# Optimization experiments

Measured on AMD Instinct MI355X. Metric: run time of the kernel, lower is better.

Reference implementation:

```python
import jax, jax.numpy as jnp
import numpy as np

EPS = 1e-12


def conv3(x, W, b):
    # x: [B,C,H,W], W: [O,I,3,3] -> SAME conv, stride 1
    y = jax.lax.conv_general_dilated(x, W, (1, 1), 'SAME',
                                     dimension_numbers=('NCHW', 'OIHW', 'NCHW'))
    return y + b[None, :, None, None]


def unfold3(x):
    # torch F.unfold(kernel=3, padding=1): [B,C,H,W] -> [B, C*9, H*W]
    B, C, H, W = x.shape
    xp = jnp.pad(x, ((0, 0), (0, 0), (1, 1), (1, 1)))
    patches = jnp.stack([xp[:, :, i:i + H, j:j + W]
                         for i in range(3) for j in range(3)], axis=2)  # [B,C,9,H,W]
    return patches.reshape(B, C * 9, H * W)


def fold3(u, H, W):
    # torch F.fold(kernel=3, padding=1): [B, C*9, H*W] -> [B,C,H,W] (overlap-add)
    B = u.shape[0]
    C = u.shape[1] // 9
    p = u.reshape(B, C, 3, 3, H, W)
    out = jnp.zeros((B, C, H + 2, W + 2), u.dtype)
    for i in range(3):
        for j in range(3):
            out = out.at[:, :, i:i + H, j:j + W].add(p[:, :, i, j])
    return out[:, :, 1:-1, 1:-1]


def l2norm(v, axis):
    n = jnp.sqrt(jnp.sum(v * v, axis=axis, keepdims=True))
    return v / jnp.maximum(n, EPS)


def setup_inputs() -> dict:
    key = jax.random.key(0)
    ks = jax.random.split(key, 10)
    in_c, q_c = 64, 32
    B, H, W = 1, 96, 96
    s = 0.05
    return {
        'x':  jax.random.normal(ks[0], (B, in_c, H, W), jnp.float32),
        'W1': jax.random.normal(ks[1], (in_c, in_c, 3, 3), jnp.float32) * s,
        'b1': jax.random.normal(ks[2], (in_c,), jnp.float32) * s,
        'W2': jax.random.normal(ks[3], (in_c, in_c, 3, 3), jnp.float32) * s,
        'b2': jax.random.normal(ks[4], (in_c,), jnp.float32) * s,
        'Wq': jax.random.normal(ks[5], (q_c, in_c, 3, 3), jnp.float32) * s,
        'bq': jax.random.normal(ks[6], (q_c,), jnp.float32) * s,
        'Wk': jax.random.normal(ks[7], (q_c, in_c, 3, 3), jnp.float32) * s,
        'bk': jax.random.normal(ks[8], (q_c,), jnp.float32) * s,
    }


def reference(x, W1, b1, W2, b2, Wq, bq, Wk, bk):
    TOPK = 5
    B, C, H, W = x.shape
    L = H * W

    feature = jax.nn.relu(conv3(jax.nn.relu(conv3(x, W1, b1)), W2, b2))
    q = conv3(x, Wq, bq)
    k = conv3(x, Wk, bk)

    q_unfold = l2norm(unfold3(q), axis=1)                      # [B, Q9, L]
    k_unfold = l2norm(jnp.swapaxes(unfold3(k), 1, 2), axis=2)  # [B, L, Q9]

    R_qk = jnp.einsum('blc,bcm->blm', k_unfold, q_unfold)      # [B, L_k, L_q]

    # topk over dim=1 (key positions) for each query position
    vals, idxs = jax.lax.top_k(jnp.swapaxes(R_qk, 1, 2), TOPK)  # [B, L_q, K]
    R_maxs = jnp.swapaxes(vals, 1, 2)                           # [B, K, L]
    R_indexs = jnp.swapaxes(idxs, 1, 2)                         # [B, K, L]

    x_unfold = unfold3(x)                                       # [B, C*9, L]
    acc = jnp.zeros_like(x)
    for i in range(1, TOPK):
        idx = R_indexs[:, i, :][:, None, :]                     # [B,1,L]
        T_unfold = jnp.take_along_axis(x_unfold, idx, axis=2)   # [B, C*9, L]
        T = fold3(T_unfold, H, W) / 9.0
        S = R_maxs[:, i, :].reshape(B, 1, H, W)
        acc = acc + T * S
    y = feature + x + acc / float(TOPK - 1)
    return y
```

## Files before the change

kernel.cpp:

```cpp
#include <hip/hip_runtime.h>
#include <math.h>

#define HH 96
#define WW 96
#define LL 9216
#define D9 288
#define TOPK 5
#define NK 6
#define NCAND 8
#define KSPLIT 32
#define CPQ (KSPLIT * NK)
#define KEYS_PER_SPLIT (LL / KSPLIT)
#define PASSES (KEYS_PER_SPLIT / 32)
#define CHUNKS (32 * 36)
#define KROW 292

typedef short short8 __attribute__((ext_vector_type(8)));
typedef float f32x16 __attribute__((ext_vector_type(16)));

__device__ __forceinline__ float  asf(unsigned u) { union { unsigned u; float f; } a; a.u = u; return a.f; }
__device__ __forceinline__ unsigned asu(float f)  { union { float f; unsigned u; } a; a.f = f; return a.u; }

__device__ __forceinline__ unsigned short f2bf(float f) {
    unsigned u = asu(f);
    unsigned r = u + 0x7fff + ((u >> 16) & 1);
    return (unsigned short)(r >> 16);
}

template<int N>
__device__ __forceinline__ void ins_med3(float* v, float x) {
    float nv[N];
    nv[0] = fmaxf(v[0], x);
    #pragma unroll
    for (int s = 1; s < N; ++s) nv[s] = __builtin_amdgcn_fmed3f(v[s-1], v[s], x);
    #pragma unroll
    for (int s = 0; s < N; ++s) v[s] = nv[s];
}

__device__ __forceinline__ bool better_tb(float av, int ai, float bv, int bi) {
    return (av > bv) || (av == bv && ai < bi);
}

template<int N>
__device__ __forceinline__ void insert_tb(float (&v)[N], int (&ix)[N], float nv, int ni) {
    if (better_tb(nv, ni, v[N-1], ix[N-1])) {
        v[N-1] = nv; ix[N-1] = ni;
        #pragma unroll
        for (int s = N-1; s > 0; --s) {
            if (better_tb(v[s], ix[s], v[s-1], ix[s-1])) {
                float tv = v[s]; v[s] = v[s-1]; v[s-1] = tv;
                int ti = ix[s]; ix[s] = ix[s-1]; ix[s-1] = ti;
            }
        }
    }
}

__device__ __forceinline__ void conv2px4co(
    const float* __restrict__ in, const float* __restrict__ Wt,
    const float* __restrict__ bias, float* __restrict__ out,
    int co0, int doRelu)
{
    int pix0 = (blockIdx.x * 256 + threadIdx.x) * 2;
    int y = pix0 / WW, x0 = pix0 - y * WW;
    bool mL = (x0 > 0), mR = (x0 < 94);

    float acc[4][2];
    #pragma unroll
    for (int j = 0; j < 4; ++j) acc[j][0] = acc[j][1] = bias[co0 + j];

    #pragma unroll 2
    for (int ci = 0; ci < 64; ++ci) {
        const float* xp = in + (size_t)ci * LL;
        float r[3][4];
        #pragma unroll
        for (int u = 0; u < 3; ++u) {
            int yy = y + u - 1;
            bool yok = (unsigned)yy < 96u;
            const float* row = xp + yy * WW + x0;
            r[u][0] = (yok && mL) ? row[-1] : 0.0f;
            r[u][1] = yok ? row[0] : 0.0f;
            r[u][2] = yok ? row[1] : 0.0f;
            r[u][3] = (yok && mR) ? row[2] : 0.0f;
        }
        const float* wb = Wt + ((size_t)co0 * 64 + ci) * 9;
        #pragma unroll
        for (int j = 0; j < 4; ++j) {
            const float* wp = wb + (size_t)j * 64 * 9;
            #pragma unroll
            for (int u = 0; u < 3; ++u)
                #pragma unroll
                for (int v = 0; v < 3; ++v) {
                    float w = wp[u*3+v];
                    acc[j][0] = fmaf(r[u][v],     w, acc[j][0]);
                    acc[j][1] = fmaf(r[u][v + 1], w, acc[j][1]);
                }
        }
    }
    #pragma unroll
    for (int j = 0; j < 4; ++j) {
        float2 o;
        o.x = doRelu ? fmaxf(acc[j][0], 0.0f) : acc[j][0];
        o.y = doRelu ? fmaxf(acc[j][1], 0.0f) : acc[j][1];
        *(float2*)(out + (size_t)(co0 + j) * LL + pix0) = o;
    }
}

__global__ __launch_bounds__(256) void conv_stage1_kernel(
    const float* __restrict__ x,
    const float* __restrict__ W1, const float* __restrict__ b1, float* __restrict__ c1,
    const float* __restrict__ Wq, const float* __restrict__ bq,
    const float* __restrict__ Wk, const float* __restrict__ bk,
    float* __restrict__ qq, float* __restrict__ kk)
{
    int g = blockIdx.y;
    if (g < 16)      conv2px4co(x, W1, b1, c1, g * 4,        1);
    else if (g < 24) conv2px4co(x, Wq, bq, qq, (g - 16) * 4, 0);
    else             conv2px4co(x, Wk, bk, kk, (g - 24) * 4, 0);
}

__global__ __launch_bounds__(256) void conv2_kernel(
    const float* __restrict__ c1, const float* __restrict__ W2,
    const float* __restrict__ b2, float* __restrict__ feat)
{
    conv2px4co(c1, W2, b2, feat, blockIdx.y * 4, 1);
}

__global__ __launch_bounds__(256) void transpose_x_kernel(
    const float* __restrict__ x, float* __restrict__ xT)
{
    __shared__ float t[64][65];
    int pix0 = blockIdx.x * 64;
    int lp = threadIdx.x & 63, cg = threadIdx.x >> 6;
    #pragma unroll
    for (int cc = 0; cc < 16; ++cc) {
        int c = cg * 16 + cc;
        t[c][lp] = x[(size_t)c * LL + pix0 + lp];
    }
    __syncthreads();
    #pragma unroll
    for (int pp = 0; pp < 16; ++pp) {
        int pl = cg * 16 + pp;
        xT[(size_t)(pix0 + pl) * 64 + lp] = t[lp][pl];
    }
}

__global__ __launch_bounds__(256) void unfold_norm_kernel(
    const float* __restrict__ qq, float* __restrict__ q_f32, unsigned short* __restrict__ q_bf,
    const float* __restrict__ kk, float* __restrict__ k_f32, unsigned short* __restrict__ k_bf)
{
    const float* in; float* o32; unsigned short* obf;
    if (blockIdx.y == 0) { in = qq; o32 = q_f32; obf = q_bf; }
    else                 { in = kk; o32 = k_f32; obf = k_bf; }

    __shared__ float tile[3][32][34];
    __shared__ float inv_s[32];
    int tid = threadIdx.x;
    int l0 = blockIdx.x * 32;
    int y = l0 / WW, xb = l0 % WW;

    #pragma unroll
    for (int j = 0; j < 13; ++j) {
        int f = j * 256 + tid;
        if (f < 3 * 32 * 34) {
            int col = f % 34, cc = (f / 34) & 31, r = f / (34 * 32);
            int yy = y + r - 1, xv = xb + col - 1;
            float val = ((unsigned)yy < 96u && (unsigned)xv < 96u)
                        ? in[(size_t)cc * LL + yy * 96 + xv] : 0.0f;
            tile[r][cc][col] = val;
        }
    }
    __syncthreads();

    {
        int pxl = tid >> 3, sub = tid & 7;
        float ss = 0.0f;
        #pragma unroll
        for (int cc = 0; cc < 4; ++cc) {
            int c = sub * 4 + cc;
            #pragma unroll
            for (int u = 0; u < 3; ++u)
                #pragma unroll
                for (int v = 0; v < 3; ++v) {
                    float val = tile[u][c][pxl + v];
                    ss = fmaf(val, val, ss);
                }
        }
        ss += __shfl_xor(ss, 1);
        ss += __shfl_xor(ss, 2);
        ss += __shfl_xor(ss, 4);
        if (sub == 0) inv_s[pxl] = 1.0f / fmaxf(sqrtf(ss), 1e-12f);
    }
    __syncthreads();

    #pragma unroll 1
    for (int it = 0; it < 9; ++it) {
        int e = it * 256 + tid;
        int pxl = e / 72, dc = e - pxl * 72;
        int l = l0 + pxl;
        float inv = inv_s[pxl];
        float4 o; float* op = &o.x;
        #pragma unroll
        for (int i = 0; i < 4; ++i) {
            int d = dc * 4 + i;
            int c = d / 9, rm = d - c * 9;
            int u = rm / 3, v = rm - u * 3;
            op[i] = tile[u][c][pxl + v] * inv;
        }
        *(float4*)(o32 + (size_t)l * D9 + dc * 4) = o;
        unsigned short b4[4];
        #pragma unroll
        for (int i = 0; i < 4; ++i) b4[i] = f2bf(op[i]);
        *(uint2*)(obf + (size_t)l * D9 + dc * 4) = *(uint2*)b4;
    }
}

__global__ __launch_bounds__(256, 2) void topk_mfma_kernel(
    const unsigned short* __restrict__ qn_bf, const unsigned short* __restrict__ kn_bf,
    float* __restrict__ valsQ)
{
    __shared__ unsigned short ks[2][32 * KROW];

    int tid  = threadIdx.x;
    int lane = tid & 63;
    int col = lane & 31, khalf = lane >> 5;
    int qtile = blockIdx.x >> 5;
    int split = blockIdx.x & 31;
    int q0w = qtile * 256 + (tid >> 6) * 64;
    int key0 = split * KEYS_PER_SPLIT;

    short8 qf[2][18];
    #pragma unroll
    for (int b = 0; b < 2; ++b) {
        const unsigned short* qrow = qn_bf + (size_t)(q0w + b*32 + col) * D9 + khalf * 8;
        #pragma unroll
        for (int dg = 0; dg < 18; ++dg)
            qf[b][dg] = *(const short8*)(qrow + dg * 16);
    }

    float lv0[NK], lv1[NK];
    #pragma unroll
    for (int s = 0; s < NK; ++s) { lv0[s] = -INFINITY; lv1[s] = -INFINITY; }

    const char* kg = (const char*)kn_bf;
    uint4 pre[5];

    #pragma unroll
    for (int c0 = 0; c0 < 5; ++c0) {
        int c = tid + c0 * 256;
        if (c < CHUNKS) {
            int key = c / 36, off = c - key * 36;
            pre[c0] = *(const uint4*)(kg + (size_t)(key0 + key) * 576 + off * 16);
        }
    }
    #pragma unroll
    for (int c0 = 0; c0 < 5; ++c0) {
        int c = tid + c0 * 256;
        if (c < CHUNKS) {
            int key = c / 36, off = c - key * 36;
            char* d = (char*)ks[0] + key * (KROW*2) + off * 16;
            *(uint2*)d       = *(uint2*)&pre[c0];
            *(uint2*)(d + 8) = *((uint2*)&pre[c0] + 1);
        }
    }
    __syncthreads();

    for (int p = 0; p < PASSES; ++p) {
        if (p + 1 < PASSES) {
            #pragma unroll
            for (int c0 = 0; c0 < 5; ++c0) {
                int c = tid + c0 * 256;
                if (c < CHUNKS) {
                    int key = c / 36, off = c - key * 36;
                    pre[c0] = *(const uint4*)(kg + (size_t)(key0 + (p+1)*32 + key) * 576 + off * 16);
                }
            }
        }

        f32x16 acc0 = {}, acc1 = {};
        const char* kb = (const char*)ks[p & 1] + (size_t)col * (KROW*2) + khalf * 16;
        #pragma unroll
        for (int dg = 0; dg < 18; ++dg) {
            short8 af;
            *(uint2*)&af       = *(const uint2*)(kb + dg * 32);
            *((uint2*)&af + 1) = *(const uint2*)(kb + dg * 32 + 8);
            acc0 = __builtin_amdgcn_mfma_f32_32x32x16_bf16(af, qf[0][dg], acc0, 0, 0, 0);
            acc1 = __builtin_amdgcn_mfma_f32_32x32x16_bf16(af, qf[1][dg], acc1, 0, 0, 0);
        }

        int lbase = p * 32 + 4 * khalf;
        #pragma unroll
        for (int r = 0; r < 16; ++r) {
            unsigned lkey = (unsigned)(lbase + (r & 3) + 8 * (r >> 2));
            ins_med3<NK>(lv0, asf((asu(acc0[r]) & 0xFFFFFE00u) | lkey));
            ins_med3<NK>(lv1, asf((asu(acc1[r]) & 0xFFFFFE00u) | lkey));
        }

        if (p + 1 < PASSES) {
            #pragma unroll
            for (int c0 = 0; c0 < 5; ++c0) {
                int c = tid + c0 * 256;
                if (c < CHUNKS) {
                    int key = c / 36, off = c - key * 36;
                    char* d = (char*)ks[(p+1) & 1] + key * (KROW*2) + off * 16;
                    *(uint2*)d       = *(uint2*)&pre[c0];
                    *(uint2*)(d + 8) = *((uint2*)&pre[c0] + 1);
                }
            }
        }
        __syncthreads();
    }

    #pragma unroll
    for (int b = 0; b < 2; ++b) {
        float* lv = b ? lv1 : lv0;
        float pv[NK];
        #pragma unroll
        for (int s = 0; s < NK; ++s) pv[s] = __shfl_xor(lv[s], 32);
        #pragma unroll
        for (int s = 0; s < NK; ++s) ins_med3<NK>(lv, pv[s]);
        if (lane < 32) {
            int q = q0w + b * 32 + col;
            float* vq = valsQ + (size_t)q * CPQ + split * NK;
            #pragma unroll
            for (int s = 0; s < NK; ++s) vq[s] = lv[s];
        }
    }
}

__global__ __launch_bounds__(256) void rerank_kernel(
    const float* __restrict__ valsQ,
    const float* __restrict__ qn_f32, const float* __restrict__ kn_f32,
    float* __restrict__ vals, int* __restrict__ idxs)
{
    int tid = threadIdx.x;
    int lane = tid & 63;
    int half = lane >> 5, l32 = lane & 31;
    int q = blockIdx.x * 8 + (tid >> 6) * 2 + half;

    const float* vq = valsQ + (size_t)q * CPQ + l32 * NK;
    float v[NK];
    #pragma unroll
    for (int s = 0; s < NK; ++s) v[s] = vq[s];

    int ckey[NCAND];
    #pragma unroll
    for (int it = 0; it < NCAND; ++it) {
        float cv = v[0];
        int cl = l32;
        #pragma unroll
        for (int st = 1; st < 32; st <<= 1) {
            float ov = __shfl_xor(cv, st);
            int ol = __shfl_xor(cl, st);
            if (ov > cv || (ov == cv && ol < cl)) { cv = ov; cl = ol; }
        }
        ckey[it] = cl * KEYS_PER_SPLIT + (int)(asu(cv) & 0x1FFu);
        if (cl == l32) {
            #pragma unroll
            for (int s = 0; s < NK-1; ++s) v[s] = v[s+1];
            v[NK-1] = -INFINITY;
        }
    }

    int r = l32 >> 2, part = l32 & 3;
    const float4* qr = (const float4*)(qn_f32 + (size_t)q * D9) + part * 18;
    const float4* kr = (const float4*)(kn_f32 + (size_t)ckey[r] * D9) + part * 18;
    float s0 = 0.f, s1 = 0.f, s2 = 0.f, s3 = 0.f;
    #pragma unroll
    for (int i2 = 0; i2 < 18; ++i2) {
        float4 a = qr[i2], b = kr[i2];
        s0 = fmaf(a.x, b.x, s0); s1 = fmaf(a.y, b.y, s1);
        s2 = fmaf(a.z, b.z, s2); s3 = fmaf(a.w, b.w, s3);
    }
    float sc = (s0 + s1) + (s2 + s3);
    sc += __shfl_xor(sc, 1);
    sc += __shfl_xor(sc, 2);

    float bv[TOPK]; int bi[TOPK];
    #pragma unroll
    for (int s = 0; s < TOPK; ++s) { bv[s] = -INFINITY; bi[s] = 0x7fffffff; }
    #pragma unroll
    for (int cc = 0; cc < NCAND; ++cc) {
        float sv = __shfl(sc, half * 32 + cc * 4);
        insert_tb<TOPK>(bv, bi, sv, ckey[cc]);
    }
    if (l32 == 0) {
        #pragma unroll
        for (int s = 0; s < TOPK; ++s) {
            vals[(size_t)s * LL + q] = bv[s];
            idxs[(size_t)s * LL + q] = bi[s];
        }
    }
}

__global__ __launch_bounds__(256) void gather_out_kernel(
    const float* __restrict__ xT, const float* __restrict__ feat,
    const float* __restrict__ vals, const int* __restrict__ idxs,
    float* __restrict__ out)
{
    int wave = threadIdx.x >> 6, lane = threadIdx.x & 63;
    int pix = blockIdx.x * 4 + wave;
    int y = pix / WW, x0 = pix - y * WW;
    float acc = 0.0f;
    #pragma unroll 1
    for (int s = 1; s < TOPK; ++s) {
        float S = vals[(size_t)s * LL + pix] * (1.0f/9.0f);
        #pragma unroll
        for (int i = 0; i < 3; ++i) {
            int qy = y + 1 - i;
            #pragma unroll
            for (int j = 0; j < 3; ++j) {
                int qx = x0 + 1 - j;
                if ((unsigned)qy < 96u && (unsigned)qx < 96u) {
                    int l = idxs[(size_t)s * LL + qy * WW + qx];
                    int yl = l / WW, xl = l - yl * WW;
                    int sy = yl + i - 1, sx = xl + j - 1;
                    if ((unsigned)sy < 96u && (unsigned)sx < 96u)
                        acc = fmaf(S, xT[(size_t)(sy * WW + sx) * 64 + lane], acc);
                }
            }
        }
    }
    out[(size_t)lane * LL + pix] = feat[(size_t)lane * LL + pix]
                                 + xT[(size_t)pix * 64 + lane] + acc * 0.25f;
}

extern "C" void kernel_launch(void* const* d_in, const int* in_sizes, int n_in,
                              void* d_out, int out_size, void* d_ws, size_t ws_size,
                              hipStream_t stream)
{
    (void)in_sizes; (void)n_in; (void)out_size; (void)ws_size;
    const float* x  = (const float*)d_in[0];
    const float* W1 = (const float*)d_in[1];
    const float* b1 = (const float*)d_in[2];
    const float* W2 = (const float*)d_in[3];
    const float* b2 = (const float*)d_in[4];
    const float* Wq = (const float*)d_in[5];
    const float* bq = (const float*)d_in[6];
    const float* Wk = (const float*)d_in[7];
    const float* bk = (const float*)d_in[8];
    float* out = (float*)d_out;

    char* p = (char*)d_ws;
    float* c1     = (float*)p;            p += (size_t)64 * LL * 4;
    float* feat   = (float*)p;            p += (size_t)64 * LL * 4;
    float* xT     = (float*)p;            p += (size_t)64 * LL * 4;
    float* qq     = (float*)p;            p += (size_t)32 * LL * 4;
    float* kk     = (float*)p;            p += (size_t)32 * LL * 4;
    float* qn_f32 = (float*)p;            p += (size_t)LL * D9 * 4;
    float* kn_f32 = (float*)p;            p += (size_t)LL * D9 * 4;
    unsigned short* qn_bf = (unsigned short*)p;  p += (size_t)LL * D9 * 2;
    unsigned short* kn_bf = (unsigned short*)p;  p += (size_t)LL * D9 * 2;
    float* valsQ  = (float*)p;            p += (size_t)LL * CPQ * 4;
    float* vals   = (float*)p;            p += (size_t)TOPK * LL * 4;
    int*   idxs   = (int*)p;              p += (size_t)TOPK * LL * 4;

    conv_stage1_kernel<<<dim3(18, 32), 256, 0, stream>>>(x, W1, b1, c1, Wq, bq, Wk, bk, qq, kk);
    unfold_norm_kernel<<<dim3(288, 2), 256, 0, stream>>>(qq, qn_f32, qn_bf, kk, kn_f32, kn_bf);
    topk_mfma_kernel<<<36 * KSPLIT, 256, 0, stream>>>(qn_bf, kn_bf, valsQ);
    conv2_kernel<<<dim3(18, 16), 256, 0, stream>>>(c1, W2, b2, feat);
    transpose_x_kernel<<<144, 256, 0, stream>>>(x, xT);
    rerank_kernel<<<LL / 8, 256, 0, stream>>>(valsQ, qn_f32, kn_f32, vals, idxs);
    gather_out_kernel<<<LL / 4, 256, 0, stream>>>(xT, feat, vals, idxs, out);
}
```

Before: 354.4 us.

## Use zero-padded inputs for convolutions with software-pipelined channel loads

```diff
diff --git a/kernel.cpp b/kernel.cpp
--- a/kernel.cpp
+++ b/kernel.cpp
@@ -4,6 +4,8 @@
 #define HH 96
 #define WW 96
 #define LL 9216
+#define PW 98
+#define PCH (PW * PW)
 #define D9 288
 #define TOPK 5
 #define NK 6
@@ -55,74 +57,144 @@
     }
 }
 
-__device__ __forceinline__ void conv2px4co(
-    const float* __restrict__ in, const float* __restrict__ Wt,
-    const float* __restrict__ bias, float* __restrict__ out,
-    int co0, int doRelu)
-{
-    int pix0 = (blockIdx.x * 256 + threadIdx.x) * 2;
+__global__ __launch_bounds__(256) void pad_init_kernel(
+    const float* __restrict__ x, float* __restrict__ xpad, float* __restrict__ c1pad)
+{
+    int e = blockIdx.x * 256 + threadIdx.x;
+    if (blockIdx.y == 1) { c1pad[e] = 0.0f; return; }
+    int c = e / PCH, rem = e - c * PCH;
+    int r = rem / PW, col = rem - r * PW;
+    float val = 0.0f;
+    if ((unsigned)(r - 1) < 96u && (unsigned)(col - 1) < 96u)
+        val = x[(size_t)c * LL + (r - 1) * WW + (col - 1)];
+    xpad[e] = val;
+}
+
+template<int NCO>
+__device__ __forceinline__ void conv_pipe(
+    const float* __restrict__ inpad, const float* __restrict__ Wt,
+    const float* __restrict__ bias, int co0,
+    float (&acc)[NCO][2])
+{
+    int t = blockIdx.x * 256 + threadIdx.x;
+    int pix0 = t * 2;
     int y = pix0 / WW, x0 = pix0 - y * WW;
-    bool mL = (x0 > 0), mR = (x0 < 94);
-
-    float acc[4][2];
-    #pragma unroll
-    for (int j = 0; j < 4; ++j) acc[j][0] = acc[j][1] = bias[co0 + j];
-
-    #pragma unroll 2
-    for (int ci = 0; ci < 64; ++ci) {
-        const float* xp = in + (size_t)ci * LL;
-        float r[3][4];
+    const float* base = inpad + y * PW + x0;
+
+    #pragma unroll
+    for (int j = 0; j < NCO; ++j) acc[j][0] = acc[j][1] = bias[co0 + j];
+
+    float2 A[3][2], B[3][2];
+    #pragma unroll
+    for (int u = 0; u < 3; ++u) {
+        A[u][0] = *(const float2*)(base + u * PW);
+        A[u][1] = *(const float2*)(base + u * PW + 2);
+    }
+
+    #pragma unroll 1
+    for (int ci = 0; ci < 64; ci += 2) {
+        const float* nb = base + (size_t)(ci + 1) * PCH;
         #pragma unroll
         for (int u = 0; u < 3; ++u) {
-            int yy = y + u - 1;
-            bool yok = (unsigned)yy < 96u;
-            const float* row = xp + yy * WW + x0;
-            r[u][0] = (yok && mL) ? row[-1] : 0.0f;
-            r[u][1] = yok ? row[0] : 0.0f;
-            r[u][2] = yok ? row[1] : 0.0f;
-            r[u][3] = (yok && mR) ? row[2] : 0.0f;
-        }
-        const float* wb = Wt + ((size_t)co0 * 64 + ci) * 9;
-        #pragma unroll
-        for (int j = 0; j < 4; ++j) {
-            const float* wp = wb + (size_t)j * 64 * 9;
-            #pragma unroll
-            for (int u = 0; u < 3; ++u)
+            B[u][0] = *(const float2*)(nb + u * PW);
+            B[u][1] = *(const float2*)(nb + u * PW + 2);
+        }
+        {
+            const float* wb = Wt + ((size_t)co0 * 64 + ci) * 9;
+            #pragma unroll
+            for (int j = 0; j < NCO; ++j) {
+                const float* wp = wb + (size_t)j * 64 * 9;
                 #pragma unroll
-                for (int v = 0; v < 3; ++v) {
-                    float w = wp[u*3+v];
-                    acc[j][0] = fmaf(r[u][v],     w, acc[j][0]);
-                    acc[j][1] = fmaf(r[u][v + 1], w, acc[j][1]);
+                for (int u = 0; u < 3; ++u) {
+                    float r0 = A[u][0].x, r1 = A[u][0].y, r2 = A[u][1].x, r3 = A[u][1].y;
+                    float w0 = wp[u*3], w1 = wp[u*3+1], w2 = wp[u*3+2];
+                    acc[j][0] = fmaf(r0, w0, acc[j][0]);
+                    acc[j][1] = fmaf(r1, w0, acc[j][1]);
+                    acc[j][0] = fmaf(r1, w1, acc[j][0]);
+                    acc[j][1] = fmaf(r2, w1, acc[j][1]);
+                    acc[j][0] = fmaf(r2, w2, acc[j][0]);
+                    acc[j][1] = fmaf(r3, w2, acc[j][1]);
                 }
-        }
-    }
-    #pragma unroll
-    for (int j = 0; j < 4; ++j) {
-        float2 o;
-        o.x = doRelu ? fmaxf(acc[j][0], 0.0f) : acc[j][0];
-        o.y = doRelu ? fmaxf(acc[j][1], 0.0f) : acc[j][1];
-        *(float2*)(out + (size_t)(co0 + j) * LL + pix0) = o;
+            }
+        }
+        if (ci + 2 < 64) {
+            const float* nb2 = base + (size_t)(ci + 2) * PCH;
+            #pragma unroll
+            for (int u = 0; u < 3; ++u) {
+                A[u][0] = *(const float2*)(nb2 + u * PW);
+                A[u][1] = *(const float2*)(nb2 + u * PW + 2);
+            }
+        }
+        {
+            const float* wb = Wt + ((size_t)co0 * 64 + (ci + 1)) * 9;
+            #pragma unroll
+            for (int j = 0; j < NCO; ++j) {
+                const float* wp = wb + (size_t)j * 64 * 9;
+                #pragma unroll
+                for (int u = 0; u < 3; ++u) {
+                    float r0 = B[u][0].x, r1 = B[u][0].y, r2 = B[u][1].x, r3 = B[u][1].y;
+                    float w0 = wp[u*3], w1 = wp[u*3+1], w2 = wp[u*3+2];
+                    acc[j][0] = fmaf(r0, w0, acc[j][0]);
+                    acc[j][1] = fmaf(r1, w0, acc[j][1]);
+                    acc[j][0] = fmaf(r1, w1, acc[j][0]);
+                    acc[j][1] = fmaf(r2, w1, acc[j][1]);
+                    acc[j][0] = fmaf(r2, w2, acc[j][0]);
+                    acc[j][1] = fmaf(r3, w2, acc[j][1]);
+                }
+            }
+        }
     }
 }
 
 __global__ __launch_bounds__(256) void conv_stage1_kernel(
-    const float* __restrict__ x,
-    const float* __restrict__ W1, const float* __restrict__ b1, float* __restrict__ c1,
+    const float* __restrict__ xpad,
+    const float* __restrict__ W1, const float* __restrict__ b1, float* __restrict__ c1pad,
     const float* __restrict__ Wq, const float* __restrict__ bq,
     const float* __restrict__ Wk, const float* __restrict__ bk,
     float* __restrict__ qq, float* __restrict__ kk)
 {
     int g = blockIdx.y;
-    if (g < 16)      conv2px4co(x, W1, b1, c1, g * 4,        1);
-    else if (g < 24) conv2px4co(x, Wq, bq, qq, (g - 16) * 4, 0);
-    else             conv2px4co(x, Wk, bk, kk, (g - 24) * 4, 0);
+    int pix0 = (blockIdx.x * 256 + threadIdx.x) * 2;
+    int y = pix0 / WW, x0 = pix0 - y * WW;
+
+    if (g < 16) {
+        float acc[4][2];
+        conv_pipe<4>(xpad, W1, b1, g * 4, acc);
+        #pragma unroll
+        for (int j = 0; j < 4; ++j) {
+            float* o = c1pad + (size_t)(g * 4 + j) * PCH + (y + 1) * PW + (x0 + 1);
+            o[0] = fmaxf(acc[j][0], 0.0f);
+            o[1] = fmaxf(acc[j][1], 0.0f);
+        }
+    } else if (g < 24) {
+        float acc[4][2];
+        conv_pipe<4>(xpad, Wq, bq, (g - 16) * 4, acc);
+        #pragma unroll
+        for (int j = 0; j < 4; ++j)
+            *(float2*)(qq + (size_t)((g - 16) * 4 + j) * LL + pix0) = make_float2(acc[j][0], acc[j][1]);
+    } else {
+        float acc[4][2];
+        conv_pipe<4>(xpad, Wk, bk, (g - 24) * 4, acc);
+        #pragma unroll
+        for (int j = 0; j < 4; ++j)
+            *(float2*)(kk + (size_t)((g - 24) * 4 + j) * LL + pix0) = make_float2(acc[j][0], acc[j][1]);
+    }
 }
 
 __global__ __launch_bounds__(256) void conv2_kernel(
-    const float* __restrict__ c1, const float* __restrict__ W2,
+    const float* __restrict__ c1pad, const float* __restrict__ W2,
     const float* __restrict__ b2, float* __restrict__ feat)
 {
-    conv2px4co(c1, W2, b2, feat, blockIdx.y * 4, 1);
+    int pix0 = (blockIdx.x * 256 + threadIdx.x) * 2;
+    float acc[2][2];
+    conv_pipe<2>(c1pad, W2, b2, blockIdx.y * 2, acc);
+    #pragma unroll
+    for (int j = 0; j < 2; ++j) {
+        float2 o;
+        o.x = fmaxf(acc[j][0], 0.0f);
+        o.y = fmaxf(acc[j][1], 0.0f);
+        *(float2*)(feat + (size_t)(blockIdx.y * 2 + j) * LL + pix0) = o;
+    }
 }
 
 __global__ __launch_bounds__(256) void transpose_x_kernel(
@@ -441,7 +513,8 @@
     float* out = (float*)d_out;
 
     char* p = (char*)d_ws;
-    float* c1     = (float*)p;            p += (size_t)64 * LL * 4;
+    float* xpad   = (float*)p;            p += (size_t)64 * PCH * 4;
+    float* c1pad  = (float*)p;            p += (size_t)64 * PCH * 4;
     float* feat   = (float*)p;            p += (size_t)64 * LL * 4;
     float* xT     = (float*)p;            p += (size_t)64 * LL * 4;
     float* qq     = (float*)p;            p += (size_t)32 * LL * 4;
@@ -454,10 +527,11 @@
     float* vals   = (float*)p;            p += (size_t)TOPK * LL * 4;
     int*   idxs   = (int*)p;              p += (size_t)TOPK * LL * 4;
 
-    conv_stage1_kernel<<<dim3(18, 32), 256, 0, stream>>>(x, W1, b1, c1, Wq, bq, Wk, bk, qq, kk);
+    pad_init_kernel<<<dim3(2401, 2), 256, 0, stream>>>(x, xpad, c1pad);
+    conv_stage1_kernel<<<dim3(18, 32), 256, 0, stream>>>(xpad, W1, b1, c1pad, Wq, bq, Wk, bk, qq, kk);
     unfold_norm_kernel<<<dim3(288, 2), 256, 0, stream>>>(qq, qn_f32, qn_bf, kk, kn_f32, kn_bf);
     topk_mfma_kernel<<<36 * KSPLIT, 256, 0, stream>>>(qn_bf, kn_bf, valsQ);
-    conv2_kernel<<<dim3(18, 16), 256, 0, stream>>>(c1, W2, b2, feat);
+    conv2_kernel<<<dim3(18, 32), 256, 0, stream>>>(c1pad, W2, b2, feat);
     transpose_x_kernel<<<144, 256, 0, stream>>>(x, xT);
     rerank_kernel<<<LL / 8, 256, 0, stream>>>(valsQ, qn_f32, kn_f32, vals, idxs);
     gather_out_kernel<<<LL / 4, 256, 0, stream>>>(xT, feat, vals, idxs, out);
```

New measurement: 289.7 us. 18.3% less time.
